# Kernel optimization log

Measured on AMD Instinct MI355X. Metric: run time of the kernel, lower is better.

## Reference

```python
import jax, jax.numpy as jnp
import numpy as np

N = 50000      # nodes
E = 400000     # directed edges (self-loops added inside reference, per PyG default)
DIN = 256
DH = 32
HEADS = 8
DOUT = 40
SLOPE = 0.2    # GATv2Conv negative_slope default


def _gatv2_layer(x, src, dst, Wl, bl, Wr, br, att, bias, heads, out_ch):
    """One GATv2Conv (concat=True). x:[n,din], src/dst:[e], att:[heads,out_ch]."""
    n = x.shape[0]
    xl = (x @ Wl + bl).reshape(n, heads, out_ch)   # source transform
    xr = (x @ Wr + br).reshape(n, heads, out_ch)   # target transform
    e = jax.nn.leaky_relu(xl[src] + xr[dst], SLOPE)          # [e, H, C]
    s = jnp.einsum('ehc,hc->eh', e, att)                     # per-edge attention logits
    smax = jax.ops.segment_max(s, dst, num_segments=n)       # stable softmax over in-edges
    ex = jnp.exp(s - smax[dst])
    denom = jax.ops.segment_sum(ex, dst, num_segments=n)
    alpha = ex / denom[dst]                                  # [e, H]
    out = jax.ops.segment_sum(alpha[:, :, None] * xl[src], dst, num_segments=n)
    return out.reshape(n, heads * out_ch) + bias


def setup_inputs() -> dict:
    key = jax.random.key(0)
    ks = jax.random.split(key, 8)
    def gl(k, shape, fan_in):
        return jax.random.normal(k, shape, jnp.float32) * np.float32(1.0 / np.sqrt(fan_in))
    return {
        'x': jax.random.normal(ks[0], (N, DIN), jnp.float32),
        'edge_index': jax.random.randint(ks[1], (2, E), 0, N, jnp.int32),
        'W1l': gl(ks[2], (DIN, HEADS * DH), DIN),
        'b1l': jnp.zeros((HEADS * DH,), jnp.float32),
        'W1r': gl(ks[3], (DIN, HEADS * DH), DIN),
        'b1r': jnp.zeros((HEADS * DH,), jnp.float32),
        'att1': gl(ks[4], (HEADS, DH), DH),
        'bias1': jnp.zeros((HEADS * DH,), jnp.float32),
        'W2l': gl(ks[5], (HEADS * DH, DOUT), HEADS * DH),
        'b2l': jnp.zeros((DOUT,), jnp.float32),
        'W2r': gl(ks[6], (HEADS * DH, DOUT), HEADS * DH),
        'b2r': jnp.zeros((DOUT,), jnp.float32),
        'att2': gl(ks[7], (1, DOUT), DOUT),
        'bias2': jnp.zeros((DOUT,), jnp.float32),
    }


def reference(x, edge_index, W1l, b1l, W1r, b1r, att1, bias1,
              W2l, b2l, W2r, b2r, att2, bias2):
    n = x.shape[0]
    loop = jnp.arange(n, dtype=edge_index.dtype)  # add_self_loops=True (PyG default)
    src = jnp.concatenate([edge_index[0], loop])
    dst = jnp.concatenate([edge_index[1], loop])
    # eval mode: F.dropout is identity; normalization='none' -> Identity
    h = _gatv2_layer(x, src, dst, W1l, b1l, W1r, b1r, att1, bias1, HEADS, DH)
    h = jax.nn.elu(h)
    out = _gatv2_layer(h, src, dst, W2l, b2l, W2r, b2r, att2, bias2, 1, DOUT)
    return jax.nn.log_softmax(out, axis=1)
```

## Files before the change

kernel.cpp:

```cpp
#include <hip/hip_runtime.h>
#include <math.h>

#define NODES 50000
#define NEDGE 400000
#define ETOT  450000
#define DIN   256
#define C1    256
#define C2    40
#define SCAN_NB ((NODES + 255) / 256)

typedef __attribute__((ext_vector_type(8))) short bfrag;
typedef __attribute__((ext_vector_type(4))) float facc;

#define GPTR(p) (const __attribute__((address_space(1))) unsigned int*)(p)
#define LPTR(p) (__attribute__((address_space(3))) unsigned int*)(p)

static __device__ __forceinline__ float bf2f(unsigned int u16) {
    unsigned int x = u16 << 16;
    float f;
    __builtin_memcpy(&f, &x, 4);
    return f;
}
static __device__ __forceinline__ float bitsf(unsigned int x) {
    float f;
    __builtin_memcpy(&f, &x, 4);
    return f;
}
static __device__ __forceinline__ unsigned short f2bf(float f) {
    unsigned int x;
    __builtin_memcpy(&x, &f, 4);
    unsigned int r = x + 0x7fffu + ((x >> 16) & 1u);
    return (unsigned short)(r >> 16);
}
static __device__ __forceinline__ float fexp2(float x) {
#if __has_builtin(__builtin_amdgcn_exp2f)
    return __builtin_amdgcn_exp2f(x);
#else
    return exp2f(x);
#endif
}

static __device__ __forceinline__ float2 pk_fma(float2 a, float2 b, float2 c) {
    float2 d;
    asm("v_pk_fma_f32 %0, %1, %2, %3" : "=v"(d) : "v"(a), "v"(b), "v"(c));
    return d;
}
static __device__ __forceinline__ float2 pk_add(float2 a, float2 b) {
    float2 d;
    asm("v_pk_add_f32 %0, %1, %2" : "=v"(d) : "v"(a), "v"(b));
    return d;
}
static __device__ __forceinline__ float2 pk_mul(float2 a, float2 b) {
    float2 d;
    asm("v_pk_mul_f32 %0, %1, %2" : "=v"(d) : "v"(a), "v"(b));
    return d;
}

__global__ __launch_bounds__(256)
void cvt_bf16(const float* __restrict__ in, unsigned short* __restrict__ out, int n8) {
    int i = blockIdx.x * 256 + threadIdx.x;
    if (i >= n8) return;
    const float4* p = (const float4*)in + (size_t)i * 2;
    float4 u0 = p[0], u1 = p[1];
    bfrag pk;
    pk[0] = (short)f2bf(u0.x); pk[1] = (short)f2bf(u0.y);
    pk[2] = (short)f2bf(u0.z); pk[3] = (short)f2bf(u0.w);
    pk[4] = (short)f2bf(u1.x); pk[5] = (short)f2bf(u1.y);
    pk[6] = (short)f2bf(u1.z); pk[7] = (short)f2bf(u1.w);
    *(bfrag*)(out + (size_t)i * 8) = pk;
}

__global__ void zero_int(int* p, int n) {
    int i = blockIdx.x * blockDim.x + threadIdx.x;
    if (i < n) p[i] = 0;
}

__global__ void count_kernel(const int* __restrict__ dstRow, int* __restrict__ cnt) {
    int e = blockIdx.x * blockDim.x + threadIdx.x;
    if (e >= ETOT) return;
    int d = (e < NEDGE) ? dstRow[e] : (e - NEDGE);
    atomicAdd(&cnt[d], 1);
}

__global__ __launch_bounds__(256)
void scan_blk(const int* __restrict__ cnt, int* __restrict__ off, int* __restrict__ blkTot) {
    __shared__ int buf[256];
    const int t = threadIdx.x;
    const int i = blockIdx.x * 256 + t;
    int v = (i < NODES) ? cnt[i] : 0;
    buf[t] = v;
    __syncthreads();
    #pragma unroll
    for (int d = 1; d < 256; d <<= 1) {
        int add = (t >= d) ? buf[t - d] : 0;
        __syncthreads();
        buf[t] += add;
        __syncthreads();
    }
    if (i < NODES) off[i] = buf[t] - v;
    if (t == 255) blkTot[blockIdx.x] = buf[255];
}

__global__ __launch_bounds__(256)
void scan_top(const int* __restrict__ blkTot, int* __restrict__ blkOff, int* __restrict__ offEnd) {
    __shared__ int buf[256];
    const int t = threadIdx.x;
    int v = (t < SCAN_NB) ? blkTot[t] : 0;
    buf[t] = v;
    __syncthreads();
    #pragma unroll
    for (int d = 1; d < 256; d <<= 1) {
        int add = (t >= d) ? buf[t - d] : 0;
        __syncthreads();
        buf[t] += add;
        __syncthreads();
    }
    if (t < SCAN_NB) blkOff[t] = buf[t] - v;
    if (t == 255) *offEnd = buf[255];
}

__global__ __launch_bounds__(256)
void scan_fix(int* __restrict__ off, int* __restrict__ wrk, const int* __restrict__ blkOff) {
    const int i = blockIdx.x * 256 + threadIdx.x;
    if (i < NODES) {
        int v = off[i] + blkOff[blockIdx.x];
        off[i] = v;
        wrk[i] = v;
    }
}

__global__ void place_kernel(const int* __restrict__ srcRow, const int* __restrict__ dstRow,
                             int* __restrict__ wrk, int* __restrict__ csr) {
    int e = blockIdx.x * blockDim.x + threadIdx.x;
    if (e >= ETOT) return;
    int d, s;
    if (e < NEDGE) { d = dstRow[e]; s = srcRow[e]; }
    else           { d = e - NEDGE; s = d; }
    int slot = atomicAdd(&wrk[d], 1);
    csr[slot] = s;
}

__global__ void prep_w(const float* __restrict__ Wl, const float* __restrict__ Wr,
                       unsigned short* __restrict__ Wt, int K, int Nhalf) {
    int idx = blockIdx.x * 256 + threadIdx.x;
    int n = idx / K;
    int k = idx - n * K;
    if (n >= 2 * Nhalf) return;
    float v = (n < Nhalf) ? Wl[(size_t)k * Nhalf + n] : Wr[(size_t)k * Nhalf + (n - Nhalf)];
    Wt[idx] = f2bf(v);
}

#define GBM 128
#define GBN 128
#define GBK 32

template<typename OUTT, bool SWZ>
__global__ __launch_bounds__(256)
void mfma_gemm(const unsigned short* __restrict__ Ab, const unsigned short* __restrict__ Bt,
               const float* __restrict__ bl, const float* __restrict__ br,
               OUTT* __restrict__ Cl, OUTT* __restrict__ Cr,
               int M, int K, int Nrows, int Nhalf, int nbnShift)
{
    __shared__ __align__(16) unsigned short As[2][GBM * GBK];
    __shared__ __align__(16) unsigned short Bs[2][GBN * GBK];

    const int tid  = threadIdx.x;
    const int lane = tid & 63;
    const int w    = tid >> 6;
    const int wr   = w >> 1;
    const int wc   = w & 1;

    int tile;
    if constexpr (SWZ) {
        const int nwg = gridDim.x;
        const int q = nwg >> 3, r = nwg & 7;
        const int xcd = blockIdx.x & 7;
        const int idx = blockIdx.x >> 3;
        tile = (xcd < r ? xcd * (q + 1) : r * (q + 1) + (xcd - r) * q) + idx;
    } else {
        tile = blockIdx.x;
    }
    const int bx   = tile >> nbnShift;
    const int by   = tile & ((1 << nbnShift) - 1);
    const int row0 = bx * GBM;
    const int col0 = by * GBN;

    facc acc[4][4];
    #pragma unroll
    for (int i = 0; i < 4; ++i)
        #pragma unroll
        for (int j = 0; j < 4; ++j) {
            facc z = {0.f, 0.f, 0.f, 0.f};
            acc[i][j] = z;
        }

    const int rA  = lane >> 2;
    const int kgA = (lane & 3) ^ ((rA >> 1) & 3);

    #define STAGE(bufi, k0)                                                     \
    {                                                                           \
        _Pragma("unroll")                                                       \
        for (int p = 0; p < 2; ++p) {                                           \
            const int chunk = p * 4 + w;                                        \
            const int r_loc = chunk * 16 + rA;                                  \
            const int ga = min(row0 + r_loc, M - 1);                            \
            __builtin_amdgcn_global_load_lds(                                   \
                GPTR(Ab + (size_t)ga * K + (k0) + kgA * 8),                     \
                LPTR(&As[bufi][chunk * 512]), 16, 0, 0);                        \
            const int gb = min(col0 + r_loc, Nrows - 1);                        \
            __builtin_amdgcn_global_load_lds(                                   \
                GPTR(Bt + (size_t)gb * K + (k0) + kgA * 8),                     \
                LPTR(&Bs[bufi][chunk * 512]), 16, 0, 0);                        \
        }                                                                       \
    }

    const int fr    = lane & 15;
    const int sRead = (lane >> 4) ^ ((fr >> 1) & 3);
    const int nt    = K / GBK;

    STAGE(0, 0);
    for (int t = 0; t < nt; ++t) {
        const int cur = t & 1;
        if (t + 1 < nt) {
            STAGE(cur ^ 1, (t + 1) * GBK);
            asm volatile("s_waitcnt vmcnt(4)" ::: "memory");
        } else {
            asm volatile("s_waitcnt vmcnt(0)" ::: "memory");
        }
        __builtin_amdgcn_s_barrier();
        __builtin_amdgcn_sched_barrier(0);

        bfrag af[4], bfv[4];
        #pragma unroll
        for (int mi = 0; mi < 4; ++mi)
            af[mi] = *(const bfrag*)(&As[cur][(wr * 64 + mi * 16 + fr) * 32 + sRead * 8]);
        #pragma unroll
        for (int ni = 0; ni < 4; ++ni)
            bfv[ni] = *(const bfrag*)(&Bs[cur][(wc * 64 + ni * 16 + fr) * 32 + sRead * 8]);
        #pragma unroll
        for (int mi = 0; mi < 4; ++mi)
            #pragma unroll
            for (int ni = 0; ni < 4; ++ni)
                acc[mi][ni] = __builtin_amdgcn_mfma_f32_16x16x32_bf16(
                    af[mi], bfv[ni], acc[mi][ni], 0, 0, 0);

        __builtin_amdgcn_s_barrier();
    }
    #undef STAGE

    #pragma unroll
    for (int mi = 0; mi < 4; ++mi) {
        const int rbase = row0 + wr * 64 + mi * 16 + ((lane >> 4) << 2);
        #pragma unroll
        for (int ni = 0; ni < 4; ++ni) {
            const int col = col0 + wc * 64 + ni * 16 + (lane & 15);
            #pragma unroll
            for (int rg = 0; rg < 4; ++rg) {
                int r = rbase + rg;
                if (r >= M) continue;
                float v = acc[mi][ni][rg];
                if (col < Nhalf) {
                    v += bl[col];
                    if constexpr (sizeof(OUTT) == 2)
                        Cl[(size_t)r * Nhalf + col] = (OUTT)f2bf(v);
                    else
                        Cl[(size_t)r * Nhalf + col] = (OUTT)v;
                } else if (col < 2 * Nhalf) {
                    int c2 = col - Nhalf;
                    v += br[c2];
                    if constexpr (sizeof(OUTT) == 2)
                        Cr[(size_t)r * Nhalf + c2] = (OUTT)f2bf(v);
                    else
                        Cr[(size_t)r * Nhalf + c2] = (OUTT)v;
                }
            }
        }
    }
}

__global__ __launch_bounds__(256)
void fused_l1(const int* __restrict__ off,
              const int* __restrict__ csr, const unsigned short* __restrict__ xl,
              const unsigned short* xr, const float* __restrict__ att,
              const float* __restrict__ bias, unsigned short* hout)
{
    const int lane = threadIdx.x & 63;
    const int n    = blockIdx.x * 4 + (threadIdx.x >> 6);
    if (n >= NODES) return;

    const int a = off[n], b = off[n + 1];

    const uint2 xrn = *(const uint2*)(xr + (size_t)n * C1 + lane * 4);
    const float2 xr01 = {bitsf(xrn.x << 16), bitsf(xrn.x & 0xffff0000u)};
    const float2 xr23 = {bitsf(xrn.y << 16), bitsf(xrn.y & 0xffff0000u)};
    const float4 wv = *(const float4*)(att + lane * 4);
    const float L2E = 1.4426950408889634f;
    const float2 w6_01 = {wv.x * (0.6f * L2E), wv.y * (0.6f * L2E)};
    const float2 w4_01 = {wv.x * (0.4f * L2E), wv.y * (0.4f * L2E)};
    const float2 w6_23 = {wv.z * (0.6f * L2E), wv.w * (0.6f * L2E)};
    const float2 w4_23 = {wv.z * (0.4f * L2E), wv.w * (0.4f * L2E)};

    float m = -INFINITY, d = 0.f;
    float2 ac01 = {0.f, 0.f}, ac23 = {0.f, 0.f};

    for (int base = a; base < b; base += 64) {
        const int cn = min(64, b - base);
        int mySrc = 0;
        if (lane < cn) mySrc = csr[base + lane];

        #define ROW1(i) (*(const uint2*)(xl + (size_t)__shfl(mySrc, min((i), cn - 1)) * C1 + lane * 4))
        #define PROC1(i, R)                                                          \
        {                                                                            \
            const float2 x01 = {bitsf((R).x << 16), bitsf((R).x & 0xffff0000u)};     \
            const float2 x23 = {bitsf((R).y << 16), bitsf((R).y & 0xffff0000u)};     \
            const float2 v01 = pk_add(x01, xr01);                                    \
            const float2 v23 = pk_add(x23, xr23);                                    \
            const float2 av01 = {fabsf(v01.x), fabsf(v01.y)};                        \
            const float2 av23 = {fabsf(v23.x), fabsf(v23.y)};                        \
            float2 p2 = pk_mul(w6_01, v01);                                          \
            p2 = pk_fma(w4_01, av01, p2);                                            \
            p2 = pk_fma(w6_23, v23, p2);                                             \
            p2 = pk_fma(w4_23, av23, p2);                                            \
            float p = p2.x + p2.y;                                                   \
            p += __shfl_xor(p, 1);                                                   \
            p += __shfl_xor(p, 2);                                                   \
            p += __shfl_xor(p, 4);                                                   \
            if (__any(p > m + 8.f)) {                                                \
                const float mN = fmaxf(m, p);                                        \
                const float sc = fexp2(m - mN);                                      \
                const float wg = fexp2(p - mN);                                      \
                m = mN;                                                              \
                d = d * sc + wg;                                                     \
                const float2 s2 = {sc, sc};                                          \
                const float2 g2 = {wg, wg};                                          \
                ac01 = pk_fma(g2, x01, pk_mul(ac01, s2));                            \
                ac23 = pk_fma(g2, x23, pk_mul(ac23, s2));                            \
            } else {                                                                 \
                const float wg = fexp2(p - m);                                       \
                d += wg;                                                             \
                const float2 g2 = {wg, wg};                                          \
                ac01 = pk_fma(g2, x01, ac01);                                        \
                ac23 = pk_fma(g2, x23, ac23);                                        \
            }                                                                        \
        }

        uint2 r0, r1, r2, r3;
        r0 = ROW1(0);
        if (1 < cn) r1 = ROW1(1);
        if (2 < cn) r2 = ROW1(2);
        if (3 < cn) r3 = ROW1(3);
        for (int i = 0; i < cn; i += 4) {
            PROC1(i, r0);
            if (i + 4 < cn) r0 = ROW1(i + 4);
            if (i + 1 < cn) {
                PROC1(i + 1, r1);
                if (i + 5 < cn) r1 = ROW1(i + 5);
            }
            if (i + 2 < cn) {
                PROC1(i + 2, r2);
                if (i + 6 < cn) r2 = ROW1(i + 6);
            }
            if (i + 3 < cn) {
                PROC1(i + 3, r3);
                if (i + 7 < cn) r3 = ROW1(i + 7);
            }
        }
        #undef ROW1
        #undef PROC1
    }

    const float inv = 1.f / d;
    const float4 bv = *(const float4*)(bias + lane * 4);
    float v0 = ac01.x * inv + bv.x, v1 = ac01.y * inv + bv.y;
    float v2 = ac23.x * inv + bv.z, v3 = ac23.y * inv + bv.w;
    v0 = v0 > 0.f ? v0 : (expf(v0) - 1.f);
    v1 = v1 > 0.f ? v1 : (expf(v1) - 1.f);
    v2 = v2 > 0.f ? v2 : (expf(v2) - 1.f);
    v3 = v3 > 0.f ? v3 : (expf(v3) - 1.f);
    uint2 o;
    o.x = (unsigned int)f2bf(v0) | ((unsigned int)f2bf(v1) << 16);
    o.y = (unsigned int)f2bf(v2) | ((unsigned int)f2bf(v3) << 16);
    *(uint2*)(hout + (size_t)n * C1 + lane * 4) = o;
}

__global__ __launch_bounds__(256)
void fused_l2(const int* __restrict__ off,
              const int* __restrict__ csr, const float* __restrict__ h2l,
              const float* __restrict__ h2r, const float* __restrict__ att,
              const float* __restrict__ bias, float* __restrict__ out)
{
    const int lane = threadIdx.x & 63;
    const int n    = blockIdx.x * 4 + (threadIdx.x >> 6);
    if (n >= NODES) return;
    const int l8 = lane & 7;
    const int g  = lane >> 3;

    const int a = off[n], b = off[n + 1];
    const float L2E = 1.4426950408889634f;

    float w6[5], w4[5], xr[5];
    #pragma unroll
    for (int j = 0; j < 5; ++j) {
        const int c = l8 + 8 * j;
        const float w = att[c];
        w6[j] = w * (0.6f * L2E);
        w4[j] = w * (0.4f * L2E);
        xr[j] = h2r[(size_t)n * C2 + c];
    }

    float m = -INFINITY, dl = 0.f;
    float acc[5] = {0.f, 0.f, 0.f, 0.f, 0.f};

    for (int base = a; base < b; base += 64) {
        const int cn = min(64, b - base);
        int mySrc = 0;
        if (lane < cn) mySrc = csr[base + lane];

        for (int c0 = 0; c0 < cn; c0 += 8) {
            const int idx = c0 + g;
            const bool active = idx < cn;
            const int src = __shfl(mySrc, min(idx, cn - 1));
            const float* row = h2l + (size_t)src * C2 + l8;
            float R[5];
            #pragma unroll
            for (int j = 0; j < 5; ++j) R[j] = row[8 * j];

            float p = 0.f;
            #pragma unroll
            for (int j = 0; j < 5; ++j) {
                const float v = R[j] + xr[j];
                p = fmaf(w6[j], v, p);
                p = fmaf(w4[j], fabsf(v), p);
            }
            p += __shfl_xor(p, 1);
            p += __shfl_xor(p, 2);
            p += __shfl_xor(p, 4);
            if (!active) p = -INFINITY;

            if (__any(p > m + 8.f)) {
                float pm = p;
                pm = fmaxf(pm, __shfl_xor(pm, 8));
                pm = fmaxf(pm, __shfl_xor(pm, 16));
                pm = fmaxf(pm, __shfl_xor(pm, 32));
                const float mN = fmaxf(m, pm);
                const float sc = fexp2(m - mN);
                const float wg = fexp2(p - mN);
                m = mN;
                dl = dl * sc + wg;
                #pragma unroll
                for (int j = 0; j < 5; ++j) acc[j] = fmaf(wg, R[j], acc[j] * sc);
            } else {
                const float wg = fexp2(p - m);
                dl += wg;
                #pragma unroll
                for (int j = 0; j < 5; ++j) acc[j] = fmaf(wg, R[j], acc[j]);
            }
        }
    }

    #pragma unroll
    for (int o = 8; o < 64; o <<= 1) {
        dl += __shfl_xor(dl, o);
        #pragma unroll
        for (int j = 0; j < 5; ++j) acc[j] += __shfl_xor(acc[j], o);
    }

    const float inv = 1.f / dl;
    float v[5];
    float mx = -INFINITY;
    #pragma unroll
    for (int j = 0; j < 5; ++j) {
        v[j] = acc[j] * inv + bias[l8 + 8 * j];
        mx = fmaxf(mx, v[j]);
    }
    mx = fmaxf(mx, __shfl_xor(mx, 1));
    mx = fmaxf(mx, __shfl_xor(mx, 2));
    mx = fmaxf(mx, __shfl_xor(mx, 4));
    float s = 0.f;
    #pragma unroll
    for (int j = 0; j < 5; ++j) s += expf(v[j] - mx);
    s += __shfl_xor(s, 1);
    s += __shfl_xor(s, 2);
    s += __shfl_xor(s, 4);
    const float lg = logf(s);
    if (g == 0) {
        #pragma unroll
        for (int j = 0; j < 5; ++j)
            out[(size_t)n * C2 + l8 + 8 * j] = v[j] - mx - lg;
    }
}

extern "C" void kernel_launch(void* const* d_in, const int* in_sizes, int n_in,
                              void* d_out, int out_size, void* d_ws, size_t ws_size,
                              hipStream_t stream)
{
    const float* x     = (const float*)d_in[0];
    const int*   ei    = (const int*)  d_in[1];
    const float* W1l   = (const float*)d_in[2];
    const float* b1l   = (const float*)d_in[3];
    const float* W1r   = (const float*)d_in[4];
    const float* b1r   = (const float*)d_in[5];
    const float* att1  = (const float*)d_in[6];
    const float* bias1 = (const float*)d_in[7];
    const float* W2l   = (const float*)d_in[8];
    const float* b2l   = (const float*)d_in[9];
    const float* W2r   = (const float*)d_in[10];
    const float* b2r   = (const float*)d_in[11];
    const float* att2  = (const float*)d_in[12];
    const float* bias2 = (const float*)d_in[13];
    float* out = (float*)d_out;

    float* ws = (float*)d_ws;
    unsigned short* xl1 = (unsigned short*)ws;
    unsigned short* xr1 = (unsigned short*)(ws + 6400000);
    unsigned short* xb  = (unsigned short*)(ws + 12800000);
    int*   csr    = (int*)(ws + 19200000);
    int*   off    = csr + ETOT;
    int*   cnt    = off + (NODES + 1);
    int*   wrk    = cnt + NODES;
    int*   blkTot = wrk + NODES;
    int*   blkOff = blkTot + SCAN_NB;
    unsigned short* Wt1 = (unsigned short*)(ws + 19810000);
    unsigned short* Wt2 = (unsigned short*)(ws + 19880000);
    unsigned short* h = xr1;
    float* h2l = ws;
    float* h2r = ws + 2000000;

    const int* srcRow = ei;
    const int* dstRow = ei + NEDGE;

    zero_int<<<(NODES + 255) / 256, 256, 0, stream>>>(cnt, NODES);
    count_kernel<<<(ETOT + 255) / 256, 256, 0, stream>>>(dstRow, cnt);
    scan_blk<<<SCAN_NB, 256, 0, stream>>>(cnt, off, blkTot);
    scan_top<<<1, 256, 0, stream>>>(blkTot, blkOff, off + NODES);
    scan_fix<<<SCAN_NB, 256, 0, stream>>>(off, wrk, blkOff);
    place_kernel<<<(ETOT + 255) / 256, 256, 0, stream>>>(srcRow, dstRow, wrk, csr);

    cvt_bf16<<<(NODES * DIN / 8 + 255) / 256, 256, 0, stream>>>(x, xb, NODES * DIN / 8);
    prep_w<<<(512 * 256 + 255) / 256, 256, 0, stream>>>(W1l, W1r, Wt1, DIN, C1);
    prep_w<<<(80 * 256 + 255) / 256, 256, 0, stream>>>(W2l, W2r, Wt2, C1, C2);

    mfma_gemm<unsigned short, true><<<((NODES + GBM - 1) / GBM) * 4, 256, 0, stream>>>(
        xb, Wt1, b1l, b1r, xl1, xr1, NODES, DIN, 2 * C1, C1, 2);
    fused_l1<<<(NODES + 3) / 4, 256, 0, stream>>>(off, csr, xl1, xr1, att1, bias1, h);

    mfma_gemm<float, false><<<(NODES + GBM - 1) / GBM, 256, 0, stream>>>(
        h, Wt2, b2l, b2r, h2l, h2r, NODES, C1, 2 * C2, C2, 0);
    fused_l2<<<(NODES + 3) / 4, 256, 0, stream>>>(off, csr, h2l, h2r, att2, bias2, out);
}
```

Baseline: 215.3 us.

## Pad CSR rows to multiples of four and load sources as int4

Each node's CSR segment is padded to a multiple of 4 entries and the CSR buffer is zero-filled, so padded slots point at node 0. The layer-1 aggregation can then read four source indices with one int4 load and gather four rows with no bounds checks, masking padded logits to -inf. Layer 2 reads source indices straight from CSR per 8-lane group instead of broadcasting them with shuffles. This removes per-chunk shuffles and branch-heavy tail handling, at the cost of wasted gathers for padding rows and an extra memset of the enlarged CSR.

```diff
diff --git a/kernel.cpp b/kernel.cpp
--- a/kernel.cpp
+++ b/kernel.cpp
@@ -8,6 +8,7 @@
 #define C1    256
 #define C2    40
 #define SCAN_NB ((NODES + 255) / 256)
+#define CSRCAP  600064
 
 typedef __attribute__((ext_vector_type(8))) short bfrag;
 typedef __attribute__((ext_vector_type(4))) float facc;
@@ -15,12 +16,6 @@
 #define GPTR(p) (const __attribute__((address_space(1))) unsigned int*)(p)
 #define LPTR(p) (__attribute__((address_space(3))) unsigned int*)(p)
 
-static __device__ __forceinline__ float bf2f(unsigned int u16) {
-    unsigned int x = u16 << 16;
-    float f;
-    __builtin_memcpy(&f, &x, 4);
-    return f;
-}
 static __device__ __forceinline__ float bitsf(unsigned int x) {
     float f;
     __builtin_memcpy(&f, &x, 4);
@@ -70,11 +65,6 @@
     *(bfrag*)(out + (size_t)i * 8) = pk;
 }
 
-__global__ void zero_int(int* p, int n) {
-    int i = blockIdx.x * blockDim.x + threadIdx.x;
-    if (i < n) p[i] = 0;
-}
-
 __global__ void count_kernel(const int* __restrict__ dstRow, int* __restrict__ cnt) {
     int e = blockIdx.x * blockDim.x + threadIdx.x;
     if (e >= ETOT) return;
@@ -87,7 +77,7 @@
     __shared__ int buf[256];
     const int t = threadIdx.x;
     const int i = blockIdx.x * 256 + t;
-    int v = (i < NODES) ? cnt[i] : 0;
+    int v = (i < NODES) ? ((cnt[i] + 3) & ~3) : 0;
     buf[t] = v;
     __syncthreads();
     #pragma unroll
@@ -279,16 +269,18 @@
 }
 
 __global__ __launch_bounds__(256)
-void fused_l1(const int* __restrict__ off,
+void fused_l1(const int* __restrict__ off, const int* __restrict__ deg,
               const int* __restrict__ csr, const unsigned short* __restrict__ xl,
-              const unsigned short* xr, const float* __restrict__ att,
-              const float* __restrict__ bias, unsigned short* hout)
+              const unsigned short* __restrict__ xr, const float* __restrict__ att,
+              const float* __restrict__ bias, unsigned short* __restrict__ hout)
 {
     const int lane = threadIdx.x & 63;
     const int n    = blockIdx.x * 4 + (threadIdx.x >> 6);
     if (n >= NODES) return;
 
-    const int a = off[n], b = off[n + 1];
+    const int a  = __builtin_amdgcn_readfirstlane(off[n]);
+    const int dn = __builtin_amdgcn_readfirstlane(deg[n]);
+    const int np = (dn + 3) & ~3;
 
     const uint2 xrn = *(const uint2*)(xr + (size_t)n * C1 + lane * 4);
     const float2 xr01 = {bitsf(xrn.x << 16), bitsf(xrn.x & 0xffff0000u)};
@@ -303,70 +295,59 @@
     float m = -INFINITY, d = 0.f;
     float2 ac01 = {0.f, 0.f}, ac23 = {0.f, 0.f};
 
-    for (int base = a; base < b; base += 64) {
-        const int cn = min(64, b - base);
-        int mySrc = 0;
-        if (lane < cn) mySrc = csr[base + lane];
-
-        #define ROW1(i) (*(const uint2*)(xl + (size_t)__shfl(mySrc, min((i), cn - 1)) * C1 + lane * 4))
-        #define PROC1(i, R)                                                          \
-        {                                                                            \
-            const float2 x01 = {bitsf((R).x << 16), bitsf((R).x & 0xffff0000u)};     \
-            const float2 x23 = {bitsf((R).y << 16), bitsf((R).y & 0xffff0000u)};     \
-            const float2 v01 = pk_add(x01, xr01);                                    \
-            const float2 v23 = pk_add(x23, xr23);                                    \
-            const float2 av01 = {fabsf(v01.x), fabsf(v01.y)};                        \
-            const float2 av23 = {fabsf(v23.x), fabsf(v23.y)};                        \
-            float2 p2 = pk_mul(w6_01, v01);                                          \
-            p2 = pk_fma(w4_01, av01, p2);                                            \
-            p2 = pk_fma(w6_23, v23, p2);                                             \
-            p2 = pk_fma(w4_23, av23, p2);                                            \
-            float p = p2.x + p2.y;                                                   \
-            p += __shfl_xor(p, 1);                                                   \
-            p += __shfl_xor(p, 2);                                                   \
-            p += __shfl_xor(p, 4);                                                   \
-            if (__any(p > m + 8.f)) {                                                \
-                const float mN = fmaxf(m, p);                                        \
-                const float sc = fexp2(m - mN);                                      \
-                const float wg = fexp2(p - mN);                                      \
-                m = mN;                                                              \
-                d = d * sc + wg;                                                     \
-                const float2 s2 = {sc, sc};                                          \
-                const float2 g2 = {wg, wg};                                          \
-                ac01 = pk_fma(g2, x01, pk_mul(ac01, s2));                            \
-                ac23 = pk_fma(g2, x23, pk_mul(ac23, s2));                            \
-            } else {                                                                 \
-                const float wg = fexp2(p - m);                                       \
-                d += wg;                                                             \
-                const float2 g2 = {wg, wg};                                          \
-                ac01 = pk_fma(g2, x01, ac01);                                        \
-                ac23 = pk_fma(g2, x23, ac23);                                        \
-            }                                                                        \
-        }
-
-        uint2 r0, r1, r2, r3;
-        r0 = ROW1(0);
-        if (1 < cn) r1 = ROW1(1);
-        if (2 < cn) r2 = ROW1(2);
-        if (3 < cn) r3 = ROW1(3);
-        for (int i = 0; i < cn; i += 4) {
-            PROC1(i, r0);
-            if (i + 4 < cn) r0 = ROW1(i + 4);
-            if (i + 1 < cn) {
-                PROC1(i + 1, r1);
-                if (i + 5 < cn) r1 = ROW1(i + 5);
+    for (int i = 0; i < np; i += 4) {
+        const int4 s4 = *(const int4*)(csr + a + i);
+        uint2 R[4];
+        R[0] = *(const uint2*)(xl + (size_t)s4.x * C1 + lane * 4);
+        R[1] = *(const uint2*)(xl + (size_t)s4.y * C1 + lane * 4);
+        R[2] = *(const uint2*)(xl + (size_t)s4.z * C1 + lane * 4);
+        R[3] = *(const uint2*)(xl + (size_t)s4.w * C1 + lane * 4);
+
+        float2 x01[4], x23[4];
+        float p[4];
+        #pragma unroll
+        for (int k = 0; k < 4; ++k) {
+            x01[k] = {bitsf(R[k].x << 16), bitsf(R[k].x & 0xffff0000u)};
+            x23[k] = {bitsf(R[k].y << 16), bitsf(R[k].y & 0xffff0000u)};
+            const float2 v01 = pk_add(x01[k], xr01);
+            const float2 v23 = pk_add(x23[k], xr23);
+            const float2 av01 = {fabsf(v01.x), fabsf(v01.y)};
+            const float2 av23 = {fabsf(v23.x), fabsf(v23.y)};
+            float2 p2 = pk_mul(w6_01, v01);
+            p2 = pk_fma(w4_01, av01, p2);
+            p2 = pk_fma(w6_23, v23, p2);
+            p2 = pk_fma(w4_23, av23, p2);
+            float pp = p2.x + p2.y;
+            pp += __shfl_xor(pp, 1);
+            pp += __shfl_xor(pp, 2);
+            pp += __shfl_xor(pp, 4);
+            p[k] = (i + k < dn) ? pp : -INFINITY;
+        }
+
+        const float pm = fmaxf(fmaxf(p[0], p[1]), fmaxf(p[2], p[3]));
+        if (__any(pm > m + 8.f)) {
+            #pragma unroll
+            for (int k = 0; k < 4; ++k) {
+                const float mN = fmaxf(m, p[k]);
+                const float sc = fexp2(m - mN);
+                const float wg = fexp2(p[k] - mN);
+                m = mN;
+                d = d * sc + wg;
+                const float2 s2 = {sc, sc};
+                const float2 g2 = {wg, wg};
+                ac01 = pk_fma(g2, x01[k], pk_mul(ac01, s2));
+                ac23 = pk_fma(g2, x23[k], pk_mul(ac23, s2));
             }
-            if (i + 2 < cn) {
-                PROC1(i + 2, r2);
-                if (i + 6 < cn) r2 = ROW1(i + 6);
+        } else {
+            #pragma unroll
+            for (int k = 0; k < 4; ++k) {
+                const float wg = fexp2(p[k] - m);
+                d += wg;
+                const float2 g2 = {wg, wg};
+                ac01 = pk_fma(g2, x01[k], ac01);
+                ac23 = pk_fma(g2, x23[k], ac23);
             }
-            if (i + 3 < cn) {
-                PROC1(i + 3, r3);
-                if (i + 7 < cn) r3 = ROW1(i + 7);
-            }
-        }
-        #undef ROW1
-        #undef PROC1
+        }
     }
 
     const float inv = 1.f / d;
@@ -384,7 +365,7 @@
 }
 
 __global__ __launch_bounds__(256)
-void fused_l2(const int* __restrict__ off,
+void fused_l2(const int* __restrict__ off, const int* __restrict__ deg,
               const int* __restrict__ csr, const float* __restrict__ h2l,
               const float* __restrict__ h2r, const float* __restrict__ att,
               const float* __restrict__ bias, float* __restrict__ out)
@@ -395,7 +376,8 @@
     const int l8 = lane & 7;
     const int g  = lane >> 3;
 
-    const int a = off[n], b = off[n + 1];
+    const int a  = __builtin_amdgcn_readfirstlane(off[n]);
+    const int dn = __builtin_amdgcn_readfirstlane(deg[n]);
     const float L2E = 1.4426950408889634f;
 
     float w6[5], w4[5], xr[5];
@@ -411,50 +393,43 @@
     float m = -INFINITY, dl = 0.f;
     float acc[5] = {0.f, 0.f, 0.f, 0.f, 0.f};
 
-    for (int base = a; base < b; base += 64) {
-        const int cn = min(64, b - base);
-        int mySrc = 0;
-        if (lane < cn) mySrc = csr[base + lane];
-
-        for (int c0 = 0; c0 < cn; c0 += 8) {
-            const int idx = c0 + g;
-            const bool active = idx < cn;
-            const int src = __shfl(mySrc, min(idx, cn - 1));
-            const float* row = h2l + (size_t)src * C2 + l8;
-            float R[5];
+    for (int c0 = 0; c0 < dn; c0 += 8) {
+        const int idx = c0 + g;
+        const int src = csr[a + idx];
+        const float* row = h2l + (size_t)src * C2 + l8;
+        float R[5];
+        #pragma unroll
+        for (int j = 0; j < 5; ++j) R[j] = row[8 * j];
+
+        float p = 0.f;
+        #pragma unroll
+        for (int j = 0; j < 5; ++j) {
+            const float v = R[j] + xr[j];
+            p = fmaf(w6[j], v, p);
+            p = fmaf(w4[j], fabsf(v), p);
+        }
+        p += __shfl_xor(p, 1);
+        p += __shfl_xor(p, 2);
+        p += __shfl_xor(p, 4);
+        if (idx >= dn) p = -INFINITY;
+
+        if (__any(p > m + 8.f)) {
+            float pm = p;
+            pm = fmaxf(pm, __shfl_xor(pm, 8));
+            pm = fmaxf(pm, __shfl_xor(pm, 16));
+            pm = fmaxf(pm, __shfl_xor(pm, 32));
+            const float mN = fmaxf(m, pm);
+            const float sc = fexp2(m - mN);
+            const float wg = fexp2(p - mN);
+            m = mN;
+            dl = dl * sc + wg;
             #pragma unroll
-            for (int j = 0; j < 5; ++j) R[j] = row[8 * j];
-
-            float p = 0.f;
+            for (int j = 0; j < 5; ++j) acc[j] = fmaf(wg, R[j], acc[j] * sc);
+        } else {
+            const float wg = fexp2(p - m);
+            dl += wg;
             #pragma unroll
-            for (int j = 0; j < 5; ++j) {
-                const float v = R[j] + xr[j];
-                p = fmaf(w6[j], v, p);
-                p = fmaf(w4[j], fabsf(v), p);
-            }
-            p += __shfl_xor(p, 1);
-            p += __shfl_xor(p, 2);
-            p += __shfl_xor(p, 4);
-            if (!active) p = -INFINITY;
-
-            if (__any(p > m + 8.f)) {
-                float pm = p;
-                pm = fmaxf(pm, __shfl_xor(pm, 8));
-                pm = fmaxf(pm, __shfl_xor(pm, 16));
-                pm = fmaxf(pm, __shfl_xor(pm, 32));
-                const float mN = fmaxf(m, pm);
-                const float sc = fexp2(m - mN);
-                const float wg = fexp2(p - mN);
-                m = mN;
-                dl = dl * sc + wg;
-                #pragma unroll
-                for (int j = 0; j < 5; ++j) acc[j] = fmaf(wg, R[j], acc[j] * sc);
-            } else {
-                const float wg = fexp2(p - m);
-                dl += wg;
-                #pragma unroll
-                for (int j = 0; j < 5; ++j) acc[j] = fmaf(wg, R[j], acc[j]);
-            }
+            for (int j = 0; j < 5; ++j) acc[j] = fmaf(wg, R[j], acc[j]);
         }
     }
 
@@ -515,13 +490,13 @@
     unsigned short* xr1 = (unsigned short*)(ws + 6400000);
     unsigned short* xb  = (unsigned short*)(ws + 12800000);
     int*   csr    = (int*)(ws + 19200000);
-    int*   off    = csr + ETOT;
+    int*   off    = csr + CSRCAP;
     int*   cnt    = off + (NODES + 1);
     int*   wrk    = cnt + NODES;
     int*   blkTot = wrk + NODES;
     int*   blkOff = blkTot + SCAN_NB;
-    unsigned short* Wt1 = (unsigned short*)(ws + 19810000);
-    unsigned short* Wt2 = (unsigned short*)(ws + 19880000);
+    unsigned short* Wt1 = (unsigned short*)(ws + 19960000);
+    unsigned short* Wt2 = (unsigned short*)(ws + 20030000);
     unsigned short* h = xr1;
     float* h2l = ws;
     float* h2r = ws + 2000000;
@@ -529,7 +504,8 @@
     const int* srcRow = ei;
     const int* dstRow = ei + NEDGE;
 
-    zero_int<<<(NODES + 255) / 256, 256, 0, stream>>>(cnt, NODES);
+    hipMemsetAsync(cnt, 0, NODES * sizeof(int), stream);
+    hipMemsetAsync(csr, 0, CSRCAP * sizeof(int), stream);
     count_kernel<<<(ETOT + 255) / 256, 256, 0, stream>>>(dstRow, cnt);
     scan_blk<<<SCAN_NB, 256, 0, stream>>>(cnt, off, blkTot);
     scan_top<<<1, 256, 0, stream>>>(blkTot, blkOff, off + NODES);
@@ -542,9 +518,9 @@
 
     mfma_gemm<unsigned short, true><<<((NODES + GBM - 1) / GBM) * 4, 256, 0, stream>>>(
         xb, Wt1, b1l, b1r, xl1, xr1, NODES, DIN, 2 * C1, C1, 2);
-    fused_l1<<<(NODES + 3) / 4, 256, 0, stream>>>(off, csr, xl1, xr1, att1, bias1, h);
+    fused_l1<<<(NODES + 3) / 4, 256, 0, stream>>>(off, cnt, csr, xl1, xr1, att1, bias1, h);
 
     mfma_gemm<float, false><<<(NODES + GBM - 1) / GBM, 256, 0, stream>>>(
         h, Wt2, b2l, b2r, h2l, h2r, NODES, C1, 2 * C2, C2, 0);
-    fused_l2<<<(NODES + 3) / 4, 256, 0, stream>>>(off, csr, h2l, h2r, att2, bias2, out);
-}
+    fused_l2<<<(NODES + 3) / 4, 256, 0, stream>>>(off, cnt, csr, h2l, h2r, att2, bias2, out);
+}
```

Result: slower. 221.0 us (+2.7%).
